# Kernel tuning notes

Measured on AMD Instinct MI355X. Metric: run time of the kernel, lower is better.

The kernel has to match this reference:

```python
import jax, jax.numpy as jnp
import numpy as np

B, N, M, V = 256, 16354, 512, 4096
S = round((N - 2) / (M - 1))  # = 32, stride of conv1d_st1_2 and conv1d_xt


def conv1d(x, w, b, stride, padding):
    # x: [B, L], w: [1, 1, K], b: [1] -> [B, L_out]
    y = jax.lax.conv_general_dilated(x[:, None, :], w, (stride,), [(padding, padding)])
    return y[:, 0, :] + b


def setup_inputs() -> dict:
    key = jax.random.key(0)
    ks = jax.random.split(key, 25)
    rn = lambda k, shape, s=0.1: (jax.random.normal(k, shape, jnp.float32) * s)
    return {
        "st1": jax.random.normal(ks[0], (B, N), jnp.float32),
        "ht1": jax.random.normal(ks[1], (B, M), jnp.float32),
        "zt": jax.random.normal(ks[2], (B, N - 1), jnp.float32),
        "da_t": jax.random.randint(ks[3], (B,), 0, N),
        "w_st1": rn(ks[4], (1, 1, 5)), "b_st1": rn(ks[5], (1,)),
        "w_st12": rn(ks[6], (1, 1, 2)), "b_st12": rn(ks[7], (1,)),
        "w_mt1": rn(ks[8], (1, 1, 3)), "b_mt1": rn(ks[9], (1,)),
        "w_xt": rn(ks[10], (1, 1, 2)), "b_xt": rn(ks[11], (1,)),
        "W_ih": rn(ks[12], (3 * M, M)), "W_hh": rn(ks[13], (3 * M, M)),
        "b_ih": rn(ks[14], (3 * M,)), "b_hh": rn(ks[15], (3 * M,)),
        "w_lht": rn(ks[16], (1, M)), "b_lht": rn(ks[17], (1,)),
        "w_lct": rn(ks[18], (1, M + 1)), "b_lct": rn(ks[19], (1,)),
        "emb": rn(ks[20], (V, N), 1.0),
    }


def reference(st1, ht1, zt, da_t, w_st1, b_st1, w_st12, b_st12, w_mt1, b_mt1,
              w_xt, b_xt, W_ih, W_hh, b_ih, b_hh, w_lht, b_lht, w_lct, b_lct, emb):
    da_f = da_t.astype(st1.dtype)[:, None]  # [B, 1]
    # Mt1_0: two chained 1-channel convs st1 [B,N] -> [B,M]
    Mt1_0 = conv1d(conv1d(st1, w_st1, b_st1, 1, 2), w_st12, b_st12, S, 0)
    Mt1 = jnp.concatenate([Mt1_0, ht1], axis=1)           # [B, 2M]
    Ht1 = conv1d(jax.nn.relu(Mt1), w_mt1, b_mt1, 2, 1)    # [B, M] (GRU h0)
    xt = conv1d(jnp.concatenate([zt, da_f], axis=1), w_xt, b_xt, S, 0)  # [B, M]
    # single-step GRU (torch gate math)
    gi = xt @ W_ih.T + b_ih
    gh = Ht1 @ W_hh.T + b_hh
    ir, iz, inn = jnp.split(gi, 3, axis=1)
    hr, hz, hn = jnp.split(gh, 3, axis=1)
    r = jax.nn.sigmoid(ir + hr)
    z = jax.nn.sigmoid(iz + hz)
    n_ = jnp.tanh(inn + r * hn)
    ht = (1.0 - z) * n_ + z * Ht1                         # [B, M]
    # index into frozen embedding: ((V-1)*sigmoid(linear(ht))).long()
    it = jnp.floor((V - 1) * jax.nn.sigmoid(ht @ w_lht.T + b_lht)[:, 0]).astype(jnp.int32)
    srt = jax.lax.stop_gradient(emb[it])                  # [B, N], no_grad in original
    ct = jax.nn.sigmoid(jnp.concatenate([ht, da_f], axis=1) @ w_lct.T + b_lct)[:, 0]  # [B]
    # vectorized per-row shift + zero-pad + scale (replaces the Python batch loop)
    idx = da_t[:, None] + jnp.arange(N)[None, :]          # [B, N]
    valid = idx < N
    shifted = jnp.where(valid, jnp.take_along_axis(st1, jnp.minimum(idx, N - 1), axis=1), 0.0)
    st = shifted * ct[:, None] + srt                      # [B, N]
    return st, ht
```

## Files before the change

kernel.cpp:

```cpp
#include <hip/hip_runtime.h>
#include <cstdint>
#include <cstddef>

constexpr int B_  = 256;
constexpr int N_  = 16354;
constexpr int M_  = 512;
constexpr int V_  = 4096;
constexpr int S_  = 32;
constexpr int G3  = 1536;

__global__ __launch_bounds__(512) void k_front(
    const float* __restrict__ st1, const float* __restrict__ ht1,
    const float* __restrict__ zt, const int* __restrict__ da_t,
    const float* __restrict__ w_st1, const float* __restrict__ b_st1,
    const float* __restrict__ w_st12, const float* __restrict__ b_st12,
    const float* __restrict__ w_mt1, const float* __restrict__ b_mt1,
    const float* __restrict__ w_xt, const float* __restrict__ b_xt,
    float* __restrict__ xt_out, float* __restrict__ ht1c_out)
{
    __shared__ float sm[2 * M_];
    const int b = blockIdx.x;
    const int j = threadIdx.x;

    const float* srow = st1 + (size_t)b * N_;

    const float w0 = w_st1[0], w1 = w_st1[1], w2 = w_st1[2], w3 = w_st1[3], w4 = w_st1[4];
    const float bs = b_st1[0];

    const int p = S_ * j;
    float x[6];
    if (j > 0 && j < M_ - 1) {
        const float2 a = *(const float2*)(srow + p - 2);
        const float2 c = *(const float2*)(srow + p);
        const float2 d = *(const float2*)(srow + p + 2);
        x[0] = a.x; x[1] = a.y; x[2] = c.x; x[3] = c.y; x[4] = d.x; x[5] = d.y;
    } else {
        #pragma unroll
        for (int k = 0; k < 6; ++k) {
            int ix = p - 2 + k;
            x[k] = (ix >= 0 && ix < N_) ? srow[ix] : 0.0f;
        }
    }
    float y0 = bs;
    y0 = fmaf(x[0], w0, y0); y0 = fmaf(x[1], w1, y0); y0 = fmaf(x[2], w2, y0);
    y0 = fmaf(x[3], w3, y0); y0 = fmaf(x[4], w4, y0);
    float y1 = bs;
    y1 = fmaf(x[1], w0, y1); y1 = fmaf(x[2], w1, y1); y1 = fmaf(x[3], w2, y1);
    y1 = fmaf(x[4], w3, y1); y1 = fmaf(x[5], w4, y1);

    const float m0 = fmaf(y0, w_st12[0], fmaf(y1, w_st12[1], b_st12[0]));
    sm[j]      = m0;
    sm[M_ + j] = ht1[(size_t)b * M_ + j];

    const float daf = (float)da_t[b];
    const float* zrow = zt + (size_t)b * (N_ - 1);
    const float u0 = zrow[S_ * j];
    const float u1 = (j == M_ - 1) ? daf : zrow[S_ * j + 1];
    xt_out[(size_t)b * M_ + j] = fmaf(u0, w_xt[0], fmaf(u1, w_xt[1], b_xt[0]));

    __syncthreads();

    const int q = 2 * j;
    float vm1 = 0.0f, v0, vp1 = 0.0f;
    if (q - 1 >= 0) { float t = sm[q - 1]; vm1 = t > 0.0f ? t : 0.0f; }
    { float t = sm[q]; v0 = t > 0.0f ? t : 0.0f; }
    if (q + 1 < 2 * M_) { float t = sm[q + 1]; vp1 = t > 0.0f ? t : 0.0f; }
    const float hv = fmaf(vm1, w_mt1[0], fmaf(v0, w_mt1[1], fmaf(vp1, w_mt1[2], b_mt1[0])));
    ht1c_out[(size_t)b * M_ + j] = hv;
}

constexpr int BMt = 64;
constexpr int BNt = 64;
constexpr int BKt = 32;
constexpr size_t GPART = (size_t)B_ * G3;

__global__ __launch_bounds__(256) void k_gemm(
    const float* __restrict__ xt, const float* __restrict__ Ht1c,
    const float* __restrict__ W_ih, const float* __restrict__ W_hh,
    float* __restrict__ g, int kper)
{
    __shared__ __align__(16) float As[BKt][BMt + 4];
    __shared__ __align__(16) float Ws[BKt][BNt + 4];

    const int t = threadIdx.x;
    const int bm0 = blockIdx.y * BMt;
    const int z = blockIdx.z;
    int n0 = blockIdx.x * BNt;

    const float* A;
    const float* W;
    float* out;
    if (n0 < G3) { A = xt;   W = W_ih; out = g + (size_t)(2 * z + 0) * GPART; }
    else         { A = Ht1c; W = W_hh; out = g + (size_t)(2 * z + 1) * GPART; n0 -= G3; }

    const int srow = t >> 2;
    const int sc4  = t & 3;

    const int tm = (t & 15) * 4;
    const int tn = (t >> 4) * 4;

    float acc[4][4];
    #pragma unroll
    for (int i = 0; i < 4; ++i)
        #pragma unroll
        for (int jj = 0; jj < 4; ++jj) acc[i][jj] = 0.0f;

    const int kbeg = z * kper;
    const int kend = kbeg + kper;

    for (int k0 = kbeg; k0 < kend; k0 += BKt) {
        {
            const float* ap = A + (size_t)(bm0 + srow) * M_ + k0 + 4 * sc4;
            const float4 f0 = *(const float4*)ap;
            const float4 f1 = *(const float4*)(ap + 16);
            As[4 * sc4 + 0][srow] = f0.x; As[4 * sc4 + 1][srow] = f0.y;
            As[4 * sc4 + 2][srow] = f0.z; As[4 * sc4 + 3][srow] = f0.w;
            As[16 + 4 * sc4 + 0][srow] = f1.x; As[16 + 4 * sc4 + 1][srow] = f1.y;
            As[16 + 4 * sc4 + 2][srow] = f1.z; As[16 + 4 * sc4 + 3][srow] = f1.w;
        }
        {
            const float* wp = W + (size_t)(n0 + srow) * M_ + k0 + 4 * sc4;
            const float4 g0 = *(const float4*)wp;
            const float4 g1 = *(const float4*)(wp + 16);
            Ws[4 * sc4 + 0][srow] = g0.x; Ws[4 * sc4 + 1][srow] = g0.y;
            Ws[4 * sc4 + 2][srow] = g0.z; Ws[4 * sc4 + 3][srow] = g0.w;
            Ws[16 + 4 * sc4 + 0][srow] = g1.x; Ws[16 + 4 * sc4 + 1][srow] = g1.y;
            Ws[16 + 4 * sc4 + 2][srow] = g1.z; Ws[16 + 4 * sc4 + 3][srow] = g1.w;
        }
        __syncthreads();

        #pragma unroll
        for (int k = 0; k < BKt; ++k) {
            const float4 a = *(const float4*)&As[k][tm];
            const float4 w = *(const float4*)&Ws[k][tn];
            acc[0][0] = fmaf(a.x, w.x, acc[0][0]); acc[0][1] = fmaf(a.x, w.y, acc[0][1]);
            acc[0][2] = fmaf(a.x, w.z, acc[0][2]); acc[0][3] = fmaf(a.x, w.w, acc[0][3]);
            acc[1][0] = fmaf(a.y, w.x, acc[1][0]); acc[1][1] = fmaf(a.y, w.y, acc[1][1]);
            acc[1][2] = fmaf(a.y, w.z, acc[1][2]); acc[1][3] = fmaf(a.y, w.w, acc[1][3]);
            acc[2][0] = fmaf(a.z, w.x, acc[2][0]); acc[2][1] = fmaf(a.z, w.y, acc[2][1]);
            acc[2][2] = fmaf(a.z, w.z, acc[2][2]); acc[2][3] = fmaf(a.z, w.w, acc[2][3]);
            acc[3][0] = fmaf(a.w, w.x, acc[3][0]); acc[3][1] = fmaf(a.w, w.y, acc[3][1]);
            acc[3][2] = fmaf(a.w, w.z, acc[3][2]); acc[3][3] = fmaf(a.w, w.w, acc[3][3]);
        }
        __syncthreads();
    }

    #pragma unroll
    for (int i = 0; i < 4; ++i) {
        float4 o;
        o.x = acc[i][0]; o.y = acc[i][1]; o.z = acc[i][2]; o.w = acc[i][3];
        *(float4*)&out[(size_t)(bm0 + tm + i) * G3 + n0 + tn] = o;
    }
}

__global__ __launch_bounds__(1024) void k_tail(
    const float* __restrict__ g, int ksplit,
    const float* __restrict__ b_ih, const float* __restrict__ b_hh,
    const float* __restrict__ Ht1c, const int* __restrict__ da_t,
    const float* __restrict__ w_lht, const float* __restrict__ b_lht,
    const float* __restrict__ w_lct, const float* __restrict__ b_lct,
    const float* __restrict__ st1, const float* __restrict__ emb,
    float* __restrict__ ht_out, float* __restrict__ st_out)
{
    __shared__ float red1[8], red2[8];
    __shared__ float s_ct;
    __shared__ int   s_it;

    const int b = blockIdx.x;
    const int o = threadIdx.x;
    const int da = da_t[b];

    if (o < M_) {
        const float* gib = g + (size_t)b * G3;
        const float* ghb = g + GPART + (size_t)b * G3;

        float ir  = gib[o];
        float iz  = gib[M_ + o];
        float inn = gib[2 * M_ + o];
        float hr  = ghb[o];
        float hz  = ghb[M_ + o];
        float hn  = ghb[2 * M_ + o];
        if (ksplit == 2) {
            const float* gib1 = gib + 2 * GPART;
            const float* ghb1 = ghb + 2 * GPART;
            ir  += gib1[o];
            iz  += gib1[M_ + o];
            inn += gib1[2 * M_ + o];
            hr  += ghb1[o];
            hz  += ghb1[M_ + o];
            hn  += ghb1[2 * M_ + o];
        }
        ir  += b_ih[o];
        iz  += b_ih[M_ + o];
        inn += b_ih[2 * M_ + o];
        hr  += b_hh[o];
        hz  += b_hh[M_ + o];
        hn  += b_hh[2 * M_ + o];

        const float r  = 1.0f / (1.0f + expf(-(ir + hr)));
        const float z  = 1.0f / (1.0f + expf(-(iz + hz)));
        const float n_ = tanhf(fmaf(r, hn, inn));
        const float hprev = Ht1c[(size_t)b * M_ + o];
        const float h = (1.0f - z) * n_ + z * hprev;

        ht_out[(size_t)b * M_ + o] = h;

        float p1 = h * w_lht[o];
        float p2 = h * w_lct[o];
        #pragma unroll
        for (int off = 32; off > 0; off >>= 1) {
            p1 += __shfl_down(p1, off);
            p2 += __shfl_down(p2, off);
        }
        const int wid = o >> 6, lane = o & 63;
        if (lane == 0) { red1[wid] = p1; red2[wid] = p2; }
    }
    __syncthreads();
    if (o == 0) {
        float s1 = 0.0f, s2 = 0.0f;
        #pragma unroll
        for (int i = 0; i < 8; ++i) { s1 += red1[i]; s2 += red2[i]; }
        const float a1 = s1 + b_lht[0];
        const float sg1 = 1.0f / (1.0f + expf(-a1));
        s_it = (int)floorf((float)(V_ - 1) * sg1);

        const float daf = (float)da;
        const float a2 = s2 + daf * w_lct[M_] + b_lct[0];
        s_ct = 1.0f / (1.0f + expf(-a2));
    }
    __syncthreads();

    const int   it = s_it;
    const float ct = s_ct;

    const float* er = emb + (size_t)it * N_;
    const float* sr = st1 + (size_t)b * N_;
    float* orow     = st_out + (size_t)b * N_;

    const float2* er2 = (const float2*)er;
    float2* orow2     = (float2*)orow;
    constexpr int H = N_ / 2;

    if ((da & 1) == 0) {
        for (int k = o; k < H; k += 1024) {
            const int i = 2 * k;
            const int idx = da + i;
            float2 sv;
            if (idx + 1 < N_)      sv = *(const float2*)(sr + idx);
            else if (idx < N_)     { sv.x = sr[idx]; sv.y = 0.0f; }
            else                   { sv.x = 0.0f; sv.y = 0.0f; }
            const float2 e = er2[k];
            float2 ov;
            ov.x = fmaf(sv.x, ct, e.x);
            ov.y = fmaf(sv.y, ct, e.y);
            orow2[k] = ov;
        }
    } else {
        for (int k = o; k < H; k += 1024) {
            const int i = 2 * k;
            const int idx = da + i;
            float2 sv;
            sv.x = (idx < N_)     ? sr[idx]     : 0.0f;
            sv.y = (idx + 1 < N_) ? sr[idx + 1] : 0.0f;
            const float2 e = er2[k];
            float2 ov;
            ov.x = fmaf(sv.x, ct, e.x);
            ov.y = fmaf(sv.y, ct, e.y);
            orow2[k] = ov;
        }
    }
}

extern "C" void kernel_launch(void* const* d_in, const int* in_sizes, int n_in,
                              void* d_out, int out_size, void* d_ws, size_t ws_size,
                              hipStream_t stream)
{
    const float* st1   = (const float*)d_in[0];
    const float* ht1   = (const float*)d_in[1];
    const float* zt    = (const float*)d_in[2];
    const int*   da_t  = (const int*)d_in[3];
    const float* w_st1 = (const float*)d_in[4];
    const float* b_st1 = (const float*)d_in[5];
    const float* w_st12= (const float*)d_in[6];
    const float* b_st12= (const float*)d_in[7];
    const float* w_mt1 = (const float*)d_in[8];
    const float* b_mt1 = (const float*)d_in[9];
    const float* w_xt  = (const float*)d_in[10];
    const float* b_xt  = (const float*)d_in[11];
    const float* W_ih  = (const float*)d_in[12];
    const float* W_hh  = (const float*)d_in[13];
    const float* b_ih  = (const float*)d_in[14];
    const float* b_hh  = (const float*)d_in[15];
    const float* w_lht = (const float*)d_in[16];
    const float* b_lht = (const float*)d_in[17];
    const float* w_lct = (const float*)d_in[18];
    const float* b_lct = (const float*)d_in[19];
    const float* emb   = (const float*)d_in[20];

    float* st_out = (float*)d_out;
    float* ht_out = (float*)d_out + (size_t)B_ * N_;

    float* ws   = (float*)d_ws;
    float* xt   = ws;
    float* Ht1c = xt + (size_t)B_ * M_;
    float* g    = Ht1c + (size_t)B_ * M_;

    const size_t need2 = (2 * (size_t)B_ * M_ + 4 * GPART) * sizeof(float);
    const int ksplit = (ws_size >= need2) ? 2 : 1;
    const int kper = M_ / ksplit;

    k_front<<<dim3(B_), dim3(M_), 0, stream>>>(
        st1, ht1, zt, da_t, w_st1, b_st1, w_st12, b_st12,
        w_mt1, b_mt1, w_xt, b_xt, xt, Ht1c);

    k_gemm<<<dim3(2 * G3 / BNt, B_ / BMt, ksplit), dim3(256), 0, stream>>>(
        xt, Ht1c, W_ih, W_hh, g, kper);

    k_tail<<<dim3(B_), dim3(1024), 0, stream>>>(
        g, ksplit, b_ih, b_hh, Ht1c, da_t,
        w_lht, b_lht, w_lct, b_lct, st1, emb, ht_out, st_out);
}
```

Before: 39.50 us.

## Retile GRU GEMM to full-batch 256x16 tiles with up to 4-way split-K

The gate GEMM is retiled so each block covers the whole batch of 256 rows and a 16-column slice of the weights. Weight rows are staged K-contiguous with vectorized float4 copies instead of transposed scalar stores. Split-K can now go up to 4 when the workspace allows, and the tail kernel sums a variable number of partials. This aims to read each weight row once and raise block count and occupancy, at the cost of reloading the activation tile per block and more partial-sum traffic in the tail.

```diff
diff --git a/kernel.cpp b/kernel.cpp
--- a/kernel.cpp
+++ b/kernel.cpp
@@ -69,23 +69,23 @@
     ht1c_out[(size_t)b * M_ + j] = hv;
 }
 
-constexpr int BMt = 64;
-constexpr int BNt = 64;
-constexpr int BKt = 32;
+constexpr int BMg = 256;
+constexpr int BNg = 16;
+constexpr int BKg = 32;
+constexpr int PA  = 36;
 constexpr size_t GPART = (size_t)B_ * G3;
 
-__global__ __launch_bounds__(256) void k_gemm(
+__global__ __launch_bounds__(256, 3) void k_gemm(
     const float* __restrict__ xt, const float* __restrict__ Ht1c,
     const float* __restrict__ W_ih, const float* __restrict__ W_hh,
     float* __restrict__ g, int kper)
 {
-    __shared__ __align__(16) float As[BKt][BMt + 4];
-    __shared__ __align__(16) float Ws[BKt][BNt + 4];
+    __shared__ __align__(16) float As[BMg][PA];
+    __shared__ __align__(16) float Ws[BNg][PA];
 
     const int t = threadIdx.x;
-    const int bm0 = blockIdx.y * BMt;
-    const int z = blockIdx.z;
-    int n0 = blockIdx.x * BNt;
+    const int z = blockIdx.y;
+    int n0 = blockIdx.x * BNg;
 
     const float* A;
     const float* W;
@@ -93,68 +93,60 @@
     if (n0 < G3) { A = xt;   W = W_ih; out = g + (size_t)(2 * z + 0) * GPART; }
     else         { A = Ht1c; W = W_hh; out = g + (size_t)(2 * z + 1) * GPART; n0 -= G3; }
 
-    const int srow = t >> 2;
-    const int sc4  = t & 3;
-
-    const int tm = (t & 15) * 4;
-    const int tn = (t >> 4) * 4;
-
-    float acc[4][4];
+    const int srow = t >> 3;
+    const int sk4  = (t & 7) * 4;
+
+    const int fm = t & 31;
+    const int fn = (t >> 5) * 2;
+
+    float acc[8][2];
     #pragma unroll
-    for (int i = 0; i < 4; ++i)
-        #pragma unroll
-        for (int jj = 0; jj < 4; ++jj) acc[i][jj] = 0.0f;
+    for (int i = 0; i < 8; ++i) { acc[i][0] = 0.0f; acc[i][1] = 0.0f; }
 
     const int kbeg = z * kper;
     const int kend = kbeg + kper;
 
-    for (int k0 = kbeg; k0 < kend; k0 += BKt) {
-        {
-            const float* ap = A + (size_t)(bm0 + srow) * M_ + k0 + 4 * sc4;
-            const float4 f0 = *(const float4*)ap;
-            const float4 f1 = *(const float4*)(ap + 16);
-            As[4 * sc4 + 0][srow] = f0.x; As[4 * sc4 + 1][srow] = f0.y;
-            As[4 * sc4 + 2][srow] = f0.z; As[4 * sc4 + 3][srow] = f0.w;
-            As[16 + 4 * sc4 + 0][srow] = f1.x; As[16 + 4 * sc4 + 1][srow] = f1.y;
-            As[16 + 4 * sc4 + 2][srow] = f1.z; As[16 + 4 * sc4 + 3][srow] = f1.w;
-        }
-        {
-            const float* wp = W + (size_t)(n0 + srow) * M_ + k0 + 4 * sc4;
-            const float4 g0 = *(const float4*)wp;
-            const float4 g1 = *(const float4*)(wp + 16);
-            Ws[4 * sc4 + 0][srow] = g0.x; Ws[4 * sc4 + 1][srow] = g0.y;
-            Ws[4 * sc4 + 2][srow] = g0.z; Ws[4 * sc4 + 3][srow] = g0.w;
-            Ws[16 + 4 * sc4 + 0][srow] = g1.x; Ws[16 + 4 * sc4 + 1][srow] = g1.y;
-            Ws[16 + 4 * sc4 + 2][srow] = g1.z; Ws[16 + 4 * sc4 + 3][srow] = g1.w;
+    for (int k0 = kbeg; k0 < kend; k0 += BKg) {
+        #pragma unroll
+        for (int i = 0; i < 8; ++i) {
+            const float4 v = *(const float4*)(A + (size_t)(srow + 32 * i) * M_ + k0 + sk4);
+            *(float4*)&As[srow + 32 * i][sk4] = v;
+        }
+        if (t < 128) {
+            const float4 v = *(const float4*)(W + (size_t)(n0 + (t >> 3)) * M_ + k0 + sk4);
+            *(float4*)&Ws[t >> 3][sk4] = v;
         }
         __syncthreads();
 
         #pragma unroll
-        for (int k = 0; k < BKt; ++k) {
-            const float4 a = *(const float4*)&As[k][tm];
-            const float4 w = *(const float4*)&Ws[k][tn];
-            acc[0][0] = fmaf(a.x, w.x, acc[0][0]); acc[0][1] = fmaf(a.x, w.y, acc[0][1]);
-            acc[0][2] = fmaf(a.x, w.z, acc[0][2]); acc[0][3] = fmaf(a.x, w.w, acc[0][3]);
-            acc[1][0] = fmaf(a.y, w.x, acc[1][0]); acc[1][1] = fmaf(a.y, w.y, acc[1][1]);
-            acc[1][2] = fmaf(a.y, w.z, acc[1][2]); acc[1][3] = fmaf(a.y, w.w, acc[1][3]);
-            acc[2][0] = fmaf(a.z, w.x, acc[2][0]); acc[2][1] = fmaf(a.z, w.y, acc[2][1]);
-            acc[2][2] = fmaf(a.z, w.z, acc[2][2]); acc[2][3] = fmaf(a.z, w.w, acc[2][3]);
-            acc[3][0] = fmaf(a.w, w.x, acc[3][0]); acc[3][1] = fmaf(a.w, w.y, acc[3][1]);
-            acc[3][2] = fmaf(a.w, w.z, acc[3][2]); acc[3][3] = fmaf(a.w, w.w, acc[3][3]);
+        for (int k4 = 0; k4 < 8; ++k4) {
+            const float4 w0 = *(const float4*)&Ws[fn][4 * k4];
+            const float4 w1 = *(const float4*)&Ws[fn + 1][4 * k4];
+            #pragma unroll
+            for (int i = 0; i < 8; ++i) {
+                const float4 a = *(const float4*)&As[fm + 32 * i][4 * k4];
+                acc[i][0] = fmaf(a.x, w0.x, acc[i][0]);
+                acc[i][0] = fmaf(a.y, w0.y, acc[i][0]);
+                acc[i][0] = fmaf(a.z, w0.z, acc[i][0]);
+                acc[i][0] = fmaf(a.w, w0.w, acc[i][0]);
+                acc[i][1] = fmaf(a.x, w1.x, acc[i][1]);
+                acc[i][1] = fmaf(a.y, w1.y, acc[i][1]);
+                acc[i][1] = fmaf(a.z, w1.z, acc[i][1]);
+                acc[i][1] = fmaf(a.w, w1.w, acc[i][1]);
+            }
         }
         __syncthreads();
     }
 
     #pragma unroll
-    for (int i = 0; i < 4; ++i) {
-        float4 o;
-        o.x = acc[i][0]; o.y = acc[i][1]; o.z = acc[i][2]; o.w = acc[i][3];
-        *(float4*)&out[(size_t)(bm0 + tm + i) * G3 + n0 + tn] = o;
+    for (int i = 0; i < 8; ++i) {
+        float2 o; o.x = acc[i][0]; o.y = acc[i][1];
+        *(float2*)&out[(size_t)(fm + 32 * i) * G3 + n0 + fn] = o;
     }
 }
 
 __global__ __launch_bounds__(1024) void k_tail(
-    const float* __restrict__ g, int ksplit,
+    const float* __restrict__ g, int zs,
     const float* __restrict__ b_ih, const float* __restrict__ b_hh,
     const float* __restrict__ Ht1c, const int* __restrict__ da_t,
     const float* __restrict__ w_lht, const float* __restrict__ b_lht,
@@ -171,24 +163,16 @@
     const int da = da_t[b];
 
     if (o < M_) {
-        const float* gib = g + (size_t)b * G3;
-        const float* ghb = g + GPART + (size_t)b * G3;
-
-        float ir  = gib[o];
-        float iz  = gib[M_ + o];
-        float inn = gib[2 * M_ + o];
-        float hr  = ghb[o];
-        float hz  = ghb[M_ + o];
-        float hn  = ghb[2 * M_ + o];
-        if (ksplit == 2) {
-            const float* gib1 = gib + 2 * GPART;
-            const float* ghb1 = ghb + 2 * GPART;
-            ir  += gib1[o];
-            iz  += gib1[M_ + o];
-            inn += gib1[2 * M_ + o];
-            hr  += ghb1[o];
-            hz  += ghb1[M_ + o];
-            hn  += ghb1[2 * M_ + o];
+        float ir = 0.f, iz = 0.f, inn = 0.f, hr = 0.f, hz = 0.f, hn = 0.f;
+        for (int zz = 0; zz < zs; ++zz) {
+            const float* gib = g + (size_t)(2 * zz + 0) * GPART + (size_t)b * G3;
+            const float* ghb = g + (size_t)(2 * zz + 1) * GPART + (size_t)b * G3;
+            ir  += gib[o];
+            iz  += gib[M_ + o];
+            inn += gib[2 * M_ + o];
+            hr  += ghb[o];
+            hz  += ghb[M_ + o];
+            hn  += ghb[2 * M_ + o];
         }
         ir  += b_ih[o];
         iz  += b_ih[M_ + o];
@@ -305,18 +289,20 @@
     float* Ht1c = xt + (size_t)B_ * M_;
     float* g    = Ht1c + (size_t)B_ * M_;
 
-    const size_t need2 = (2 * (size_t)B_ * M_ + 4 * GPART) * sizeof(float);
-    const int ksplit = (ws_size >= need2) ? 2 : 1;
-    const int kper = M_ / ksplit;
+    const size_t base = 2 * (size_t)B_ * M_ * sizeof(float);
+    int zs = 1;
+    if (ws_size >= base + 8 * GPART * sizeof(float))      zs = 4;
+    else if (ws_size >= base + 4 * GPART * sizeof(float)) zs = 2;
+    const int kper = M_ / zs;
 
     k_front<<<dim3(B_), dim3(M_), 0, stream>>>(
         st1, ht1, zt, da_t, w_st1, b_st1, w_st12, b_st12,
         w_mt1, b_mt1, w_xt, b_xt, xt, Ht1c);
 
-    k_gemm<<<dim3(2 * G3 / BNt, B_ / BMt, ksplit), dim3(256), 0, stream>>>(
+    k_gemm<<<dim3(2 * G3 / BNg, zs), dim3(256), 0, stream>>>(
         xt, Ht1c, W_ih, W_hh, g, kper);
 
     k_tail<<<dim3(B_), dim3(1024), 0, stream>>>(
-        g, ksplit, b_ih, b_hh, Ht1c, da_t,
+        g, zs, b_ih, b_hh, Ht1c, da_t,
         w_lht, b_lht, w_lct, b_lct, st1, emb, ht_out, st_out);
 }
```

Measured after the change: 43.57 us. +10.3%, slower.
